# Performance work log

Measured on AMD Instinct MI355X. Metric: run time of the kernel, lower is better.

The kernel has to match this reference:

```python
import jax, jax.numpy as jnp
import numpy as np

K = 3
K2 = K * K
PAD = (K - 1) // 2
DECAY_RATE = 4.0
REL_THRESHOLD = 0.3
EPS = 1e-8


def _deform_sample(depth, offset):
    """Deformable bilinear gather equivalent to the fixed-identity-weight
    ModulatedDeformConv2d (mask=1, bias=0). Returns [B, K2, H, W]."""
    B, _, H, W = depth.shape
    d = depth[:, 0]  # [B, H, W]
    dt = depth.dtype
    # mmcv offset layout: channel 2*i = dy, 2*i+1 = dx for kernel point i
    off = offset.reshape(B, K2, 2, H, W)
    off_y, off_x = off[:, :, 0], off[:, :, 1]          # [B, K2, H, W]
    ky = (jnp.arange(K2) // K - PAD).astype(dt)        # [K2]
    kx = (jnp.arange(K2) % K - PAD).astype(dt)
    ys = jnp.arange(H, dtype=dt)
    xs = jnp.arange(W, dtype=dt)
    # sampling locations: p = base_pixel + kernel_offset + learned_offset
    py = off_y + ys[None, None, :, None] + ky[None, :, None, None]  # [B,K2,H,W]
    px = off_x + xs[None, None, None, :] + kx[None, :, None, None]
    y0 = jnp.floor(py)
    x0 = jnp.floor(px)
    wy = py - y0  # bilinear weights
    wx = px - x0
    y0i = y0.astype(jnp.int32)
    x0i = x0.astype(jnp.int32)

    def gather(iy, ix):
        # zero-padded gather (matches mmcv out-of-bounds handling)
        valid = (iy >= 0) & (iy < H) & (ix >= 0) & (ix < W)
        iyc = jnp.clip(iy, 0, H - 1)
        ixc = jnp.clip(ix, 0, W - 1)
        vals = jax.vmap(lambda img, a, b: img[a, b])(d, iyc, ixc)  # [B,K2,H,W]
        return jnp.where(valid, vals, jnp.zeros((), dt))

    v00 = gather(y0i, x0i)
    v01 = gather(y0i, x0i + 1)
    v10 = gather(y0i + 1, x0i)
    v11 = gather(y0i + 1, x0i + 1)
    return (v00 * (1 - wy) * (1 - wx) + v01 * (1 - wy) * wx
            + v10 * wy * (1 - wx) + v11 * wy * wx)


def setup_inputs() -> dict:
    key = jax.random.key(0)
    k1, k2 = jax.random.split(key)
    B, H, W = 8, 480, 640
    depth = jax.random.uniform(k1, (B, 1, H, W), dtype=jnp.float32)
    offset = jax.random.normal(k2, (B, 2 * K2, H, W), dtype=jnp.float32)
    return {"depth": depth, "offset": offset}


def reference(depth, offset):
    sampled = _deform_sample(depth, offset)           # [B, K2, H, W]
    center = sampled[:, K2 // 2: K2 // 2 + 1]         # [B, 1, H, W]
    depth_diff = jnp.abs(sampled - center)
    # normalize_mode == 'threshold' (default path)
    relative_diff = depth_diff / (center + EPS)
    within = relative_diff <= REL_THRESHOLD
    affinity = jnp.exp(-DECAY_RATE * (depth_diff - center * REL_THRESHOLD))
    return jnp.where(within, jnp.ones_like(affinity), affinity)
```

## Files before the change

### kernel.cpp

```cpp
#include <hip/hip_runtime.h>

constexpr int KK = 3;
constexpr int K2 = 9;
constexpr int PADC = 1;
constexpr float DECAY = 4.0f;
constexpr float RELT = 0.3f;
constexpr float EPSV = 1e-8f;
constexpr int H = 480;
constexpr int W = 640;
constexpr int HW = H * W;

typedef float f32x4 __attribute__((ext_vector_type(4)));

constexpr int TH = 16;
constexpr int TW = 64;
constexpr int PADT = 8;
constexpr int LR = TH + 2 * PADT;
constexpr int LC = TW + 2 * PADT;
constexpr int LSTRIDE = LC + 1;
constexpr int NSTAGE = LR * LC;

__device__ __forceinline__ float dsample(const float* __restrict__ img, int iy, int ix) {
    bool valid = (iy >= 0) & (iy < H) & (ix >= 0) & (ix < W);
    int iyc = min(max(iy, 0), H - 1);
    int ixc = min(max(ix, 0), W - 1);
    float v = img[iyc * W + ixc];
    return valid ? v : 0.0f;
}

__device__ __forceinline__ void tap4(const float* __restrict__ tile,
                                     const float* __restrict__ dimg,
                                     int by0, int bx0, int r, int col,
                                     f32x4 oy, f32x4 ox, int ky, int kx,
                                     float* s4) {
    int y0[4], x0[4];
    float wy[4], wx[4];
    bool fast = true;
#pragma unroll
    for (int j = 0; j < 4; ++j) {
        float pyt = oy[j] + (float)(r + PADT + ky);
        float pxt = ox[j] + (float)(col + j + PADT + kx);
        float y0f = floorf(pyt);
        float x0f = floorf(pxt);
        wy[j] = pyt - y0f;
        wx[j] = pxt - x0f;
        y0[j] = (int)y0f;
        x0[j] = (int)x0f;
        fast &= ((unsigned)y0[j] < (unsigned)(LR - 1)) & ((unsigned)x0[j] < (unsigned)(LC - 1));
    }
    if (fast) {
#pragma unroll
        for (int j = 0; j < 4; ++j) {
            int a = y0[j] * LSTRIDE + x0[j];
            float v00 = tile[a];
            float v01 = tile[a + 1];
            float v10 = tile[a + LSTRIDE];
            float v11 = tile[a + LSTRIDE + 1];
            float h0 = fmaf(wx[j], v01 - v00, v00);
            float h1 = fmaf(wx[j], v11 - v10, v10);
            s4[j] = fmaf(wy[j], h1 - h0, h0);
        }
    } else {
#pragma unroll
        for (int j = 0; j < 4; ++j) {
            int gy = y0[j] + by0 - PADT;
            int gx = x0[j] + bx0 - PADT;
            float v00 = dsample(dimg, gy, gx);
            float v01 = dsample(dimg, gy, gx + 1);
            float v10 = dsample(dimg, gy + 1, gx);
            float v11 = dsample(dimg, gy + 1, gx + 1);
            float h0 = fmaf(wx[j], v01 - v00, v00);
            float h1 = fmaf(wx[j], v11 - v10, v10);
            s4[j] = fmaf(wy[j], h1 - h0, h0);
        }
    }
}

__global__ __launch_bounds__(256) void affinity_kernel(
    const float* __restrict__ depth,
    const float* __restrict__ offset,
    float* __restrict__ out)
{
    const int bx0 = blockIdx.x * TW;
    const int by0 = blockIdx.y * TH;
    const int b   = blockIdx.z;
    const int t   = threadIdx.x;

    __shared__ float tile[LR * LSTRIDE];

    const float* __restrict__ dimg = depth + (size_t)b * HW;

    const int col = (t & 15) * 4;
    const int r   = t >> 4;
    const int y   = by0 + r;
    const int x   = bx0 + col;

    const size_t obase = ((size_t)b * 2 * K2) * HW + (size_t)y * W + x;
    const float* __restrict__ offp = offset + obase;

    constexpr int ORD[K2] = {4, 0, 1, 2, 3, 5, 6, 7, 8};

    f32x4 oyb[2], oxb[2];
    oyb[0] = *reinterpret_cast<const f32x4*>(offp + (size_t)(2 * ORD[0]) * HW);
    oxb[0] = *reinterpret_cast<const f32x4*>(offp + (size_t)(2 * ORD[0] + 1) * HW);
    oyb[1] = *reinterpret_cast<const f32x4*>(offp + (size_t)(2 * ORD[1]) * HW);
    oxb[1] = *reinterpret_cast<const f32x4*>(offp + (size_t)(2 * ORD[1] + 1) * HW);

#pragma unroll
    for (int i = 0; i < NSTAGE / 256; ++i) {
        int idx = t + i * 256;
        int rr = idx / LC;
        int cc = idx - rr * LC;
        int yi = by0 - PADT + rr;
        int xi = bx0 - PADT + cc;
        float v = 0.0f;
        if ((unsigned)yi < (unsigned)H && (unsigned)xi < (unsigned)W)
            v = dimg[yi * W + xi];
        tile[rr * LSTRIDE + cc] = v;
    }
    __syncthreads();

    float* __restrict__ outp = out + ((size_t)b * K2) * HW + (size_t)y * W + x;

    float c4[4], thr[4], cr[4];

#pragma unroll
    for (int i = 0; i < K2; ++i) {
        const int k = ORD[i];
        f32x4 oyc = oyb[i & 1];
        f32x4 oxc = oxb[i & 1];
        if (i + 2 < K2) {
            oyb[i & 1] = *reinterpret_cast<const f32x4*>(offp + (size_t)(2 * ORD[i + 2]) * HW);
            oxb[i & 1] = *reinterpret_cast<const f32x4*>(offp + (size_t)(2 * ORD[i + 2] + 1) * HW);
        }

        float s4[4];
        tap4(tile, dimg, by0, bx0, r, col, oyc, oxc, k / KK - PADC, k % KK - PADC, s4);

        if (i == 0) {
#pragma unroll
            for (int j = 0; j < 4; ++j) {
                c4[j]  = s4[j];
                thr[j] = RELT * (s4[j] + EPSV);
                cr[j]  = RELT * s4[j];
            }
            f32x4 ones = {1.0f, 1.0f, 1.0f, 1.0f};
            __builtin_nontemporal_store(ones, reinterpret_cast<f32x4*>(outp + (size_t)4 * HW));
        } else {
            f32x4 vals;
#pragma unroll
            for (int j = 0; j < 4; ++j) {
                float diff = fabsf(s4[j] - c4[j]);
                float aff = __expf(-DECAY * (diff - cr[j]));
                vals[j] = (diff <= thr[j]) ? 1.0f : aff;
            }
            __builtin_nontemporal_store(vals, reinterpret_cast<f32x4*>(outp + (size_t)k * HW));
        }
    }
}

extern "C" void kernel_launch(void* const* d_in, const int* in_sizes, int n_in,
                              void* d_out, int out_size, void* d_ws, size_t ws_size,
                              hipStream_t stream) {
    const float* depth = (const float*)d_in[0];
    const float* offset = (const float*)d_in[1];
    float* out = (float*)d_out;

    int B = in_sizes[0] / HW;
    dim3 grid(W / TW, H / TH, B);
    affinity_kernel<<<grid, 256, 0, stream>>>(depth, offset, out);
}
```

Measured before the change: 50.53 us.

## Split kernel taps across two blocks per image to double grid parallelism

Each block now processes only half of the tap channels (0-3 or 5-8) plus the center tap, and the grid is doubled along z. The aim is more blocks and less serial work per thread to improve latency hiding. In exchange, both halves stage the same shared-memory tile, read the center offset channels twice, and recompute the center sample. Offset prefetch depth is also reduced from two taps ahead to one.

```diff
diff --git a/kernel.cpp b/kernel.cpp
--- a/kernel.cpp
+++ b/kernel.cpp
@@ -81,10 +81,11 @@
     const float* __restrict__ offset,
     float* __restrict__ out)
 {
-    const int bx0 = blockIdx.x * TW;
-    const int by0 = blockIdx.y * TH;
-    const int b   = blockIdx.z;
-    const int t   = threadIdx.x;
+    const int bx0  = blockIdx.x * TW;
+    const int by0  = blockIdx.y * TH;
+    const int b    = blockIdx.z >> 1;
+    const int half = blockIdx.z & 1;
+    const int t    = threadIdx.x;
 
     __shared__ float tile[LR * LSTRIDE];
 
@@ -98,13 +99,12 @@
     const size_t obase = ((size_t)b * 2 * K2) * HW + (size_t)y * W + x;
     const float* __restrict__ offp = offset + obase;
 
-    constexpr int ORD[K2] = {4, 0, 1, 2, 3, 5, 6, 7, 8};
+    constexpr int NCH = 5;
+    const int chbase = half ? 5 : 0;
+#define ORD(i) ((i) == 0 ? 4 : chbase + (i) - 1)
 
-    f32x4 oyb[2], oxb[2];
-    oyb[0] = *reinterpret_cast<const f32x4*>(offp + (size_t)(2 * ORD[0]) * HW);
-    oxb[0] = *reinterpret_cast<const f32x4*>(offp + (size_t)(2 * ORD[0] + 1) * HW);
-    oyb[1] = *reinterpret_cast<const f32x4*>(offp + (size_t)(2 * ORD[1]) * HW);
-    oxb[1] = *reinterpret_cast<const f32x4*>(offp + (size_t)(2 * ORD[1] + 1) * HW);
+    f32x4 oyc = *reinterpret_cast<const f32x4*>(offp + (size_t)(2 * 4) * HW);
+    f32x4 oxc = *reinterpret_cast<const f32x4*>(offp + (size_t)(2 * 4 + 1) * HW);
 
 #pragma unroll
     for (int i = 0; i < NSTAGE / 256; ++i) {
@@ -125,13 +125,13 @@
     float c4[4], thr[4], cr[4];
 
 #pragma unroll
-    for (int i = 0; i < K2; ++i) {
-        const int k = ORD[i];
-        f32x4 oyc = oyb[i & 1];
-        f32x4 oxc = oxb[i & 1];
-        if (i + 2 < K2) {
-            oyb[i & 1] = *reinterpret_cast<const f32x4*>(offp + (size_t)(2 * ORD[i + 2]) * HW);
-            oxb[i & 1] = *reinterpret_cast<const f32x4*>(offp + (size_t)(2 * ORD[i + 2] + 1) * HW);
+    for (int i = 0; i < NCH; ++i) {
+        const int k = ORD(i);
+        f32x4 oyn, oxn;
+        if (i + 1 < NCH) {
+            const int kn = ORD(i + 1);
+            oyn = *reinterpret_cast<const f32x4*>(offp + (size_t)(2 * kn) * HW);
+            oxn = *reinterpret_cast<const f32x4*>(offp + (size_t)(2 * kn + 1) * HW);
         }
 
         float s4[4];
@@ -144,8 +144,10 @@
                 thr[j] = RELT * (s4[j] + EPSV);
                 cr[j]  = RELT * s4[j];
             }
-            f32x4 ones = {1.0f, 1.0f, 1.0f, 1.0f};
-            __builtin_nontemporal_store(ones, reinterpret_cast<f32x4*>(outp + (size_t)4 * HW));
+            if (half == 0) {
+                f32x4 ones = {1.0f, 1.0f, 1.0f, 1.0f};
+                __builtin_nontemporal_store(ones, reinterpret_cast<f32x4*>(outp + (size_t)4 * HW));
+            }
         } else {
             f32x4 vals;
 #pragma unroll
@@ -156,7 +158,10 @@
             }
             __builtin_nontemporal_store(vals, reinterpret_cast<f32x4*>(outp + (size_t)k * HW));
         }
+        oyc = oyn;
+        oxc = oxn;
     }
+#undef ORD
 }
 
 extern "C" void kernel_launch(void* const* d_in, const int* in_sizes, int n_in,
@@ -167,6 +172,6 @@
     float* out = (float*)d_out;
 
     int B = in_sizes[0] / HW;
-    dim3 grid(W / TW, H / TH, B);
+    dim3 grid(W / TW, H / TH, 2 * B);
     affinity_kernel<<<grid, 256, 0, stream>>>(depth, offset, out);
 }
```

Result: slower. 56.48 us (+11.8%).
